# Performance work log

Hardware: AMD Instinct MI355X
Metric: run time of the kernel (lower is better)

Reference implementation:

```python
import jax, jax.numpy as jnp
import numpy as np

N = 8192
F_IN = 128
D = 128
NEG_SLOPE = 0.2  # cfg.negativeslope (standard GAT value)
MASK_FILL = -9e15


def setup_inputs() -> dict:
    key = jax.random.key(0)
    k1, k2, k3, k4 = jax.random.split(key, 4)
    A = jax.random.randint(k1, (N, N), 0, 2, dtype=jnp.int32)
    X = jax.random.normal(k2, (N, F_IN), dtype=jnp.float32)
    # glorot init for Ws, xavier_uniform(gain=1.414) for a
    lim_w = float(np.sqrt(6.0 / (F_IN + D)))
    Ws = jax.random.uniform(k3, (F_IN, D), minval=-lim_w, maxval=lim_w, dtype=jnp.float32)
    lim_a = 1.414 * float(np.sqrt(6.0 / (2 * D + 1)))
    a = jax.random.uniform(k4, (2 * D, 1), minval=-lim_a, maxval=lim_a, dtype=jnp.float32)
    return {"A": A, "X": X, "Ws": Ws, "a": a}


def reference(A, X, Ws, a):
    # Wh: [N, D]
    Wh = X @ Ws
    d = Wh.shape[-1]
    # additive attention: e_ij = leaky_relu(Wh_i . a1 + Wh_j . a2)
    e1 = Wh @ a[:d]          # [N, 1]
    e2 = Wh @ a[d:]          # [N, 1]
    e = jax.nn.leaky_relu(e1 + e2.T, negative_slope=NEG_SLOPE)  # [N, N]
    e = jnp.where(A > 0, e, MASK_FILL)
    attn = jax.nn.softmax(e, axis=1)  # row-wise over neighbors
    H = attn @ Wh            # [N, D]
    return H
```

## Files before the change

### kernel.cpp

```cpp
#include <hip/hip_runtime.h>
#include <hip/hip_bf16.h>

#define NN 8192
#define DD 128

typedef __attribute__((ext_vector_type(8))) short short8;
typedef __attribute__((ext_vector_type(4))) float f32x4;
typedef unsigned int u32;

__device__ __forceinline__ ushort f2bf(float f) {
    __hip_bfloat16 h = __float2bfloat16(f);
    return *(ushort*)&h;
}
__device__ __forceinline__ float asf(u32 u) {
    union { u32 i; float f; } v; v.i = u; return v.f;
}
__device__ __forceinline__ u32 asu(float f) {
    union { float f; u32 i; } v; v.f = f; return v.i;
}

__global__ __launch_bounds__(256) void k1_fused(
    const float* __restrict__ X, const float* __restrict__ Ws,
    const float* __restrict__ a, ushort* __restrict__ WhT,
    float* __restrict__ C1, float* __restrict__ C1s, u32* __restrict__ E2bf) {
    __shared__ float lWs[128 * 132];
    __shared__ float lX[32 * 132];
    __shared__ float la[256];
    int t = threadIdx.x, bx = blockIdx.x;
    int i0 = bx * 32;
    const float4* Ws4 = (const float4*)Ws;
    const float4* X4 = (const float4*)X;
    la[t] = a[t];
    for (int j = 0; j < 16; ++j) {
        int u = j * 256 + t;
        int k = u >> 5, c4 = u & 31;
        *(float4*)&lWs[k * 132 + c4 * 4] = Ws4[u];
    }
    for (int j = 0; j < 4; ++j) {
        int u = j * 256 + t;
        int r = u >> 5, c4 = u & 31;
        *(float4*)&lX[r * 132 + c4 * 4] = X4[bx * 1024 + u];
    }
    __syncthreads();
    int r0 = (t >> 5) * 4, c0 = (t & 31) * 4;
    float acc[4][4];
#pragma unroll
    for (int i = 0; i < 4; ++i)
#pragma unroll
        for (int j = 0; j < 4; ++j) acc[i][j] = 0.f;
#pragma unroll 4
    for (int k = 0; k < 128; ++k) {
        float4 wv = *(const float4*)&lWs[k * 132 + c0];
        float x0 = lX[(r0 + 0) * 132 + k];
        float x1 = lX[(r0 + 1) * 132 + k];
        float x2 = lX[(r0 + 2) * 132 + k];
        float x3 = lX[(r0 + 3) * 132 + k];
#pragma unroll
        for (int j = 0; j < 4; ++j) {
            acc[0][j] += x0 * ((const float*)&wv)[j];
            acc[1][j] += x1 * ((const float*)&wv)[j];
            acc[2][j] += x2 * ((const float*)&wv)[j];
            acc[3][j] += x3 * ((const float*)&wv)[j];
        }
    }
    __syncthreads();
    float* lT = lWs;
#pragma unroll
    for (int i = 0; i < 4; ++i)
#pragma unroll
        for (int j = 0; j < 4; ++j) lT[(c0 + j) * 33 + r0 + i] = acc[i][j];
    __syncthreads();
    if (t < 128) {
        int r = t >> 2, q = t & 3;
        float s1 = 0.f, s2 = 0.f;
        for (int j = 0; j < 32; ++j) {
            int d = q * 32 + j;
            float v = lT[d * 33 + r];
            s1 += v * la[d];
            s2 += v * la[128 + d];
        }
        s1 += __shfl_xor(s1, 1); s1 += __shfl_xor(s1, 2);
        s2 += __shfl_xor(s2, 1); s2 += __shfl_xor(s2, 2);
        if (q == 0) {
            int i = i0 + r;
            C1[i]  = __expf(s1);
            C1s[i] = __expf(0.2f * s1);
            u32 pe = (u32)f2bf(__expf(s2));
            u32 ne = (u32)f2bf(__expf(0.2f * s2));
            E2bf[i] = pe | (ne << 16);
        }
    }
    int d = t >> 1, hf = t & 1;
    __attribute__((aligned(16))) ushort tmp[16];
#pragma unroll
    for (int s = 0; s < 16; ++s) tmp[s] = f2bf(lT[d * 33 + hf * 16 + s]);
    uint4* dst = (uint4*)&WhT[(size_t)d * NN + i0 + hf * 16];
    const uint4* srcv = (const uint4*)tmp;
    dst[0] = srcv[0];
    dst[1] = srcv[1];
}

__global__ __launch_bounds__(512, 4) void k3_main(
    const int* __restrict__ A, const ushort* __restrict__ WhT,
    const float* __restrict__ C1, const float* __restrict__ C1s,
    const u32* __restrict__ E2bf, float* __restrict__ Hp,
    float* __restrict__ Lp) {

    __shared__ u32 lE[2048];

    int tid = threadIdx.x;
    int lane = tid & 63;
    int wv = tid >> 6;
    int g = wv & 3;
    int h = wv >> 2;
    int n = lane & 15;
    int kg = lane >> 4;

    int bx = blockIdx.x;
    int kb = blockIdx.y;
    int row = bx * 64 + g * 16 + n;
    int kbase = kb * 2048;

#pragma unroll
    for (int j = 0; j < 4; ++j) lE[tid + j * 512] = E2bf[kbase + tid + j * 512];

    float c1 = C1[row], c1s = C1s[row];
    const int* Arow = A + (size_t)row * NN + kbase + kg * 8;
    const ushort* Bc0 = WhT + (size_t)(h * 64 +  0 + n) * NN + kbase + kg * 8;
    const ushort* Bc1 = WhT + (size_t)(h * 64 + 16 + n) * NN + kbase + kg * 8;
    const ushort* Bc2 = WhT + (size_t)(h * 64 + 32 + n) * NN + kbase + kg * 8;
    const ushort* Bc3 = WhT + (size_t)(h * 64 + 48 + n) * NN + kbase + kg * 8;

    short8 ones;
#pragma unroll
    for (int j = 0; j < 8; ++j) ones[j] = (short)0x3F80;

    f32x4 acc0 = (f32x4){0.f, 0.f, 0.f, 0.f};
    f32x4 acc1 = (f32x4){0.f, 0.f, 0.f, 0.f};
    f32x4 acc2 = (f32x4){0.f, 0.f, 0.f, 0.f};
    f32x4 acc3 = (f32x4){0.f, 0.f, 0.f, 0.f};
    f32x4 accl = (f32x4){0.f, 0.f, 0.f, 0.f};

    __syncthreads();

    int4 Ar[2][4];
    Ar[0][0] = *(const int4*)(Arow);
    Ar[0][1] = *(const int4*)(Arow + 4);
    Ar[0][2] = *(const int4*)(Arow + 32);
    Ar[0][3] = *(const int4*)(Arow + 36);

#pragma unroll 2
    for (int kt = 0; kt < 32; ++kt) {
        int b = kt & 1;
        int ko = kt * 64;
        short8 B00 = *(const short8*)(Bc0 + ko);
        short8 B10 = *(const short8*)(Bc1 + ko);
        short8 B20 = *(const short8*)(Bc2 + ko);
        short8 B30 = *(const short8*)(Bc3 + ko);
        short8 B01 = *(const short8*)(Bc0 + ko + 32);
        short8 B11 = *(const short8*)(Bc1 + ko + 32);
        short8 B21 = *(const short8*)(Bc2 + ko + 32);
        short8 B31 = *(const short8*)(Bc3 + ko + 32);
        if (kt < 31) {
            Ar[b ^ 1][0] = *(const int4*)(Arow + ko + 64);
            Ar[b ^ 1][1] = *(const int4*)(Arow + ko + 68);
            Ar[b ^ 1][2] = *(const int4*)(Arow + ko + 96);
            Ar[b ^ 1][3] = *(const int4*)(Arow + ko + 100);
        }
#pragma unroll
        for (int tp = 0; tp < 2; ++tp) {
            int ke = ko + tp * 32 + kg * 8;
            uint4 e0 = *(const uint4*)&lE[ke];
            uint4 e1 = *(const uint4*)&lE[ke + 4];
            int am[8]; u32 ev[8];
            *(int4*)(am) = Ar[b][tp * 2];
            *(int4*)(am + 4) = Ar[b][tp * 2 + 1];
            *(uint4*)(ev) = e0; *(uint4*)(ev + 4) = e1;
            u32 wb[8];
#pragma unroll
            for (int u = 0; u < 8; ++u) {
                float ep = asf(ev[u] << 16);
                float en = asf(ev[u] & 0xFFFF0000u);
                float w = fmaxf(c1 * ep, c1s * en);
                w = am[u] ? w : 0.f;
                wb[u] = asu(w);
            }
            short8 af;
#pragma unroll
            for (int p = 0; p < 4; ++p)
                ((u32*)&af)[p] = __builtin_amdgcn_perm(wb[2 * p + 1], wb[2 * p], 0x07060302);
            acc0 = __builtin_amdgcn_mfma_f32_16x16x32_bf16(af, tp ? B01 : B00, acc0, 0, 0, 0);
            acc1 = __builtin_amdgcn_mfma_f32_16x16x32_bf16(af, tp ? B11 : B10, acc1, 0, 0, 0);
            acc2 = __builtin_amdgcn_mfma_f32_16x16x32_bf16(af, tp ? B21 : B20, acc2, 0, 0, 0);
            acc3 = __builtin_amdgcn_mfma_f32_16x16x32_bf16(af, tp ? B31 : B30, acc3, 0, 0, 0);
            if (h == 0)
                accl = __builtin_amdgcn_mfma_f32_16x16x32_bf16(af, ones, accl, 0, 0, 0);
        }
    }

    if (h == 0 && n == 0) {
#pragma unroll
        for (int r = 0; r < 4; ++r)
            Lp[(size_t)kb * NN + bx * 64 + g * 16 + kg * 4 + r] = accl[r];
    }
    float* Hpb = Hp + (size_t)kb * (NN * DD);
#pragma unroll
    for (int r = 0; r < 4; ++r) {
        int orow = bx * 64 + g * 16 + kg * 4 + r;
        Hpb[(size_t)orow * DD + h * 64 + n]      = acc0[r];
        Hpb[(size_t)orow * DD + h * 64 + 16 + n] = acc1[r];
        Hpb[(size_t)orow * DD + h * 64 + 32 + n] = acc2[r];
        Hpb[(size_t)orow * DD + h * 64 + 48 + n] = acc3[r];
    }
}

__global__ void k4_final(const float* __restrict__ Hp, const float* __restrict__ Lp,
                         float* __restrict__ out) {
    int idx = blockIdx.x * 256 + threadIdx.x;
    int i = idx >> 7;
    float sv = Hp[idx] + Hp[1048576 + idx] + Hp[2097152 + idx] + Hp[3145728 + idx];
    float l = Lp[i] + Lp[8192 + i] + Lp[16384 + i] + Lp[24576 + i];
    out[idx] = sv / l;
}

extern "C" void kernel_launch(void* const* d_in, const int* in_sizes, int n_in,
                              void* d_out, int out_size, void* d_ws, size_t ws_size,
                              hipStream_t stream) {
    const int*   A  = (const int*)d_in[0];
    const float* X  = (const float*)d_in[1];
    const float* Ws = (const float*)d_in[2];
    const float* a  = (const float*)d_in[3];
    float* out = (float*)d_out;

    char* ws = (char*)d_ws;
    ushort* WhT  = (ushort*)(ws);
    float*  C1   = (float*)(ws + (2u << 20));
    float*  C1s  = (float*)(ws + (2u << 20) + (32u << 10));
    u32*    E2bf = (u32*)(ws + (2u << 20) + (64u << 10));
    float*  Lp   = (float*)(ws + (2u << 20) + (96u << 10));
    float*  Hp   = (float*)(ws + (4u << 20));

    k1_fused<<<256, 256, 0, stream>>>(X, Ws, a, WhT, C1, C1s, E2bf);
    k3_main<<<dim3(128, 4), 512, 0, stream>>>(A, WhT, C1, C1s, E2bf, Hp, Lp);
    k4_final<<<4096, 256, 0, stream>>>(Hp, Lp, out);
}
```

Before: 476.0 us.

## Pre-pack adjacency matrix into bitmask before attention-aggregation kernel

Adds a streaming pre-pass that compresses the int32 adjacency matrix into one bit per edge. The main MFMA kernel then reads 64-bit masks per row slice instead of wide int4 loads, which cuts its global traffic and register pressure. The neighbour exponentials are also kept as separate fp32 arrays in LDS instead of packed bf16 pairs. The cost is an extra full pass over A, one more kernel launch, and twice as many LDS reads.

```diff
diff --git a/kernel.cpp b/kernel.cpp
--- a/kernel.cpp
+++ b/kernel.cpp
@@ -7,22 +7,37 @@
 typedef __attribute__((ext_vector_type(8))) short short8;
 typedef __attribute__((ext_vector_type(4))) float f32x4;
 typedef unsigned int u32;
+typedef unsigned long long u64;
 
 __device__ __forceinline__ ushort f2bf(float f) {
     __hip_bfloat16 h = __float2bfloat16(f);
     return *(ushort*)&h;
 }
-__device__ __forceinline__ float asf(u32 u) {
-    union { u32 i; float f; } v; v.i = u; return v.f;
-}
 __device__ __forceinline__ u32 asu(float f) {
     union { float f; u32 i; } v; v.f = f; return v.i;
+}
+
+__global__ __launch_bounds__(256) void k0_pack(const int* __restrict__ A,
+                                               u32* __restrict__ Abits) {
+    int t = threadIdx.x;
+    size_t base = (size_t)blockIdx.x * 8192 + (size_t)t * 32;
+    u32 bits = 0;
+#pragma unroll
+    for (int j = 0; j < 8; ++j) {
+        int4 v = *(const int4*)(A + base + j * 4);
+        bits |= (v.x != 0 ? 1u : 0u) << (j * 4 + 0);
+        bits |= (v.y != 0 ? 1u : 0u) << (j * 4 + 1);
+        bits |= (v.z != 0 ? 1u : 0u) << (j * 4 + 2);
+        bits |= (v.w != 0 ? 1u : 0u) << (j * 4 + 3);
+    }
+    Abits[blockIdx.x * 256 + t] = bits;
 }
 
 __global__ __launch_bounds__(256) void k1_fused(
     const float* __restrict__ X, const float* __restrict__ Ws,
     const float* __restrict__ a, ushort* __restrict__ WhT,
-    float* __restrict__ C1, float* __restrict__ C1s, u32* __restrict__ E2bf) {
+    float* __restrict__ C1, float* __restrict__ C1s,
+    float* __restrict__ E2p, float* __restrict__ E2n) {
     __shared__ float lWs[128 * 132];
     __shared__ float lX[32 * 132];
     __shared__ float la[256];
@@ -85,9 +100,8 @@
             int i = i0 + r;
             C1[i]  = __expf(s1);
             C1s[i] = __expf(0.2f * s1);
-            u32 pe = (u32)f2bf(__expf(s2));
-            u32 ne = (u32)f2bf(__expf(0.2f * s2));
-            E2bf[i] = pe | (ne << 16);
+            E2p[i] = __expf(s2);
+            E2n[i] = __expf(0.2f * s2);
         }
     }
     int d = t >> 1, hf = t & 1;
@@ -101,12 +115,13 @@
 }
 
 __global__ __launch_bounds__(512, 4) void k3_main(
-    const int* __restrict__ A, const ushort* __restrict__ WhT,
+    const u32* __restrict__ Abits, const ushort* __restrict__ WhT,
     const float* __restrict__ C1, const float* __restrict__ C1s,
-    const u32* __restrict__ E2bf, float* __restrict__ Hp,
-    float* __restrict__ Lp) {
-
-    __shared__ u32 lE[2048];
+    const float* __restrict__ E2p, const float* __restrict__ E2n,
+    float* __restrict__ Hp, float* __restrict__ Lp) {
+
+    __shared__ float lEp[2048];
+    __shared__ float lEn[2048];
 
     int tid = threadIdx.x;
     int lane = tid & 63;
@@ -122,10 +137,13 @@
     int kbase = kb * 2048;
 
 #pragma unroll
-    for (int j = 0; j < 4; ++j) lE[tid + j * 512] = E2bf[kbase + tid + j * 512];
+    for (int j = 0; j < 4; ++j) {
+        lEp[tid + j * 512] = E2p[kbase + tid + j * 512];
+        lEn[tid + j * 512] = E2n[kbase + tid + j * 512];
+    }
 
     float c1 = C1[row], c1s = C1s[row];
-    const int* Arow = A + (size_t)row * NN + kbase + kg * 8;
+    const u64* Arow = (const u64*)Abits + (size_t)row * 128 + kb * 32;
     const ushort* Bc0 = WhT + (size_t)(h * 64 +  0 + n) * NN + kbase + kg * 8;
     const ushort* Bc1 = WhT + (size_t)(h * 64 + 16 + n) * NN + kbase + kg * 8;
     const ushort* Bc2 = WhT + (size_t)(h * 64 + 32 + n) * NN + kbase + kg * 8;
@@ -143,15 +161,11 @@
 
     __syncthreads();
 
-    int4 Ar[2][4];
-    Ar[0][0] = *(const int4*)(Arow);
-    Ar[0][1] = *(const int4*)(Arow + 4);
-    Ar[0][2] = *(const int4*)(Arow + 32);
-    Ar[0][3] = *(const int4*)(Arow + 36);
+    u64 bits_cur = Arow[0];
+    int shft = kg * 8;
 
 #pragma unroll 2
     for (int kt = 0; kt < 32; ++kt) {
-        int b = kt & 1;
         int ko = kt * 64;
         short8 B00 = *(const short8*)(Bc0 + ko);
         short8 B10 = *(const short8*)(Bc1 + ko);
@@ -161,28 +175,25 @@
         short8 B11 = *(const short8*)(Bc1 + ko + 32);
         short8 B21 = *(const short8*)(Bc2 + ko + 32);
         short8 B31 = *(const short8*)(Bc3 + ko + 32);
-        if (kt < 31) {
-            Ar[b ^ 1][0] = *(const int4*)(Arow + ko + 64);
-            Ar[b ^ 1][1] = *(const int4*)(Arow + ko + 68);
-            Ar[b ^ 1][2] = *(const int4*)(Arow + ko + 96);
-            Ar[b ^ 1][3] = *(const int4*)(Arow + ko + 100);
-        }
+        u64 bits_nxt = 0;
+        if (kt < 31) bits_nxt = Arow[kt + 1];
+        u32 lo = (u32)bits_cur, hi = (u32)(bits_cur >> 32);
 #pragma unroll
         for (int tp = 0; tp < 2; ++tp) {
             int ke = ko + tp * 32 + kg * 8;
-            uint4 e0 = *(const uint4*)&lE[ke];
-            uint4 e1 = *(const uint4*)&lE[ke + 4];
-            int am[8]; u32 ev[8];
-            *(int4*)(am) = Ar[b][tp * 2];
-            *(int4*)(am + 4) = Ar[b][tp * 2 + 1];
-            *(uint4*)(ev) = e0; *(uint4*)(ev + 4) = e1;
+            float4 p0 = *(const float4*)&lEp[ke];
+            float4 p1 = *(const float4*)&lEp[ke + 4];
+            float4 n0 = *(const float4*)&lEn[ke];
+            float4 n1 = *(const float4*)&lEn[ke + 4];
+            u32 byte = ((tp ? hi : lo) >> shft) & 0xFFu;
+            float ep[8], en[8];
+            *(float4*)(ep) = p0; *(float4*)(ep + 4) = p1;
+            *(float4*)(en) = n0; *(float4*)(en + 4) = n1;
             u32 wb[8];
 #pragma unroll
             for (int u = 0; u < 8; ++u) {
-                float ep = asf(ev[u] << 16);
-                float en = asf(ev[u] & 0xFFFF0000u);
-                float w = fmaxf(c1 * ep, c1s * en);
-                w = am[u] ? w : 0.f;
+                float w = fmaxf(c1 * ep[u], c1s * en[u]);
+                w = (byte & (1u << u)) ? w : 0.f;
                 wb[u] = asu(w);
             }
             short8 af;
@@ -196,6 +207,7 @@
             if (h == 0)
                 accl = __builtin_amdgcn_mfma_f32_16x16x32_bf16(af, ones, accl, 0, 0, 0);
         }
+        bits_cur = bits_nxt;
     }
 
     if (h == 0 && n == 0) {
@@ -233,14 +245,17 @@
     float* out = (float*)d_out;
 
     char* ws = (char*)d_ws;
-    ushort* WhT  = (ushort*)(ws);
-    float*  C1   = (float*)(ws + (2u << 20));
-    float*  C1s  = (float*)(ws + (2u << 20) + (32u << 10));
-    u32*    E2bf = (u32*)(ws + (2u << 20) + (64u << 10));
-    float*  Lp   = (float*)(ws + (2u << 20) + (96u << 10));
-    float*  Hp   = (float*)(ws + (4u << 20));
-
-    k1_fused<<<256, 256, 0, stream>>>(X, Ws, a, WhT, C1, C1s, E2bf);
-    k3_main<<<dim3(128, 4), 512, 0, stream>>>(A, WhT, C1, C1s, E2bf, Hp, Lp);
+    u32*    Abits = (u32*)(ws);
+    ushort* WhT   = (ushort*)(ws + (8u << 20));
+    float*  C1    = (float*)(ws + (10u << 20));
+    float*  C1s   = (float*)(ws + (10u << 20) + (32u << 10));
+    float*  E2p   = (float*)(ws + (10u << 20) + (64u << 10));
+    float*  E2n   = (float*)(ws + (10u << 20) + (96u << 10));
+    float*  Lp    = (float*)(ws + (10u << 20) + (128u << 10));
+    float*  Hp    = (float*)(ws + (12u << 20));
+
+    k0_pack<<<8192, 256, 0, stream>>>(A, Abits);
+    k1_fused<<<256, 256, 0, stream>>>(X, Ws, a, WhT, C1, C1s, E2p, E2n);
+    k3_main<<<dim3(128, 4), 512, 0, stream>>>(Abits, WhT, C1, C1s, E2p, E2n, Hp, Lp);
     k4_final<<<4096, 256, 0, stream>>>(Hp, Lp, out);
 }
```

New measurement: 506.0 us. 1.06x slower.
